# Kernel optimization log

Hardware: AMD Instinct MI355X
Metric: run time of the kernel (lower is better)

## Reference

```python
import jax, jax.numpy as jnp
import numpy as np

COST_CLASS, COST_BBOX, COST_GIOU = 1.0, 5.0, 2.0
BS, Q, K, T = 16, 1024, 256, 128


def setup_inputs() -> dict:
    key = jax.random.key(0)
    k1, k2, k3, k4 = jax.random.split(key, 4)
    pred_logits = jax.random.normal(k1, (BS, Q, K), dtype=jnp.float32)
    # predicted boxes in (mid, width) format, width > 0
    pred_boxes = jax.random.uniform(k2, (BS, Q, 2), dtype=jnp.float32, minval=0.05, maxval=1.0)
    # target boxes in (x0, x1) format with x0 < x1
    tgt_boxes = jnp.sort(jax.random.uniform(k3, (BS, T, 2), dtype=jnp.float32), axis=-1)
    tgt_labels = jax.random.randint(k4, (BS, T), 0, K, dtype=jnp.int32)
    return {"pred_logits": pred_logits, "pred_boxes": pred_boxes,
            "tgt_boxes": tgt_boxes, "tgt_labels": tgt_labels}


def midwtoxy(x):
    mid, w = x[..., 0], x[..., 1]
    return jnp.stack([mid - 0.5 * w, mid + 0.5 * w], axis=-1)


def getgiou(b1, b2):
    # b1: [N,2] (x0,x1), b2: [M,2]; returns [N,M] generalized IoU for 1-D intervals
    area1 = b1[:, 1] - b1[:, 0]              # [N]
    area2 = b2[:, 1] - b2[:, 0]              # [M]
    lt = jnp.maximum(b1[:, None, 0], b2[None, :, 0])
    rb = jnp.minimum(b1[:, None, 1], b2[None, :, 1])
    inter = jnp.clip(rb - lt, 0.0)           # [N,M]
    union = area1[:, None] + area2[None, :] - inter
    iou = inter / union
    hull_lt = jnp.minimum(b1[:, None, 0], b2[None, :, 0])
    hull_rb = jnp.maximum(b1[:, None, 1], b2[None, :, 1])
    hull = jnp.clip(hull_rb - hull_lt, 0.0)
    return iou - (hull - union) / hull


def reference(pred_logits, pred_boxes, tgt_boxes, tgt_labels):
    bs, q, k = pred_logits.shape
    out_prob = jax.nn.softmax(pred_logits.reshape(bs * q, k), axis=-1)  # [bs*Q, K]
    out_bbox = midwtoxy(pred_boxes.reshape(bs * q, 2))                  # [bs*Q, 2] (x0,x1)
    tgt_bbox = tgt_boxes.reshape(-1, 2)                                 # [bs*T, 2]
    tgt_ids = tgt_labels.reshape(-1)                                    # [bs*T]

    cost_class = -out_prob[:, tgt_ids]                                  # [bs*Q, bs*T]
    # L1 cdist over 2 coords, without materializing a [N,M,2] tensor
    cost_bbox = (jnp.abs(out_bbox[:, None, 0] - tgt_bbox[None, :, 0]) +
                 jnp.abs(out_bbox[:, None, 1] - tgt_bbox[None, :, 1]))
    cost_giou = -getgiou(out_bbox, tgt_bbox)

    C = COST_BBOX * cost_bbox + COST_CLASS * cost_class + COST_GIOU * cost_giou
    # [bs, Q, bs*T]; the original feeds the per-sample diagonal blocks
    # C[b, :, b*T:(b+1)*T] to scipy linear_sum_assignment (CPU, non-differentiable,
    # excluded from this GPU-math baseline).
    return C.reshape(bs, q, -1)
```

## Files before the change

### kernel.cpp

```cpp
#include <hip/hip_runtime.h>

#define BS 16
#define Q  1024
#define K  256
#define T  128
#define NROWS (BS * Q)
#define M     (BS * T)
#define RPB   4

__device__ __forceinline__ float cost_fn(float x0, float x1, float w1,
                                         float tx0, float tx1, float p) {
    float l1   = fabsf(x0 - tx0) + fabsf(x1 - tx1);
    float ir   = fminf(x1, tx1) - fmaxf(x0, tx0);
    float s    = w1 + (tx1 - tx0);
    float inter= fmaxf(ir, 0.0f);
    float mn   = fminf(ir, 0.0f);
    float uni  = s - inter;
    float hull = s - ir;
    float giou = (inter * hull + mn * uni) * __builtin_amdgcn_rcpf(uni * hull);
    return fmaf(5.0f, l1, -p) - 2.0f * giou;
}

__global__ __launch_bounds__(256) void hungarian_cost_kernel(
    const float* __restrict__ pred_logits,
    const float* __restrict__ pred_boxes,
    const float* __restrict__ tgt_boxes,
    const int*   __restrict__ tgt_labels,
    float* __restrict__ out)
{
    __shared__ float probs[RPB][K];

    const int t    = threadIdx.x;
    const int w    = t >> 6;
    const int lane = t & 63;
    const int n    = blockIdx.x * RPB + w;

    const float4* lg4 = (const float4*)(pred_logits + (size_t)n * K);
    float4 v = lg4[lane];
    float e0 = __expf(v.x), e1 = __expf(v.y), e2 = __expf(v.z), e3 = __expf(v.w);
    float sum = (e0 + e1) + (e2 + e3);
    #pragma unroll
    for (int off = 1; off < 64; off <<= 1)
        sum += __shfl_xor(sum, off, 64);
    float rs = __builtin_amdgcn_rcpf(sum);

    float4* pr4 = (float4*)&probs[w][0];
    float4 pv; pv.x = e0 * rs; pv.y = e1 * rs; pv.z = e2 * rs; pv.w = e3 * rs;
    pr4[lane] = pv;

    float mid = pred_boxes[(size_t)n * 2 + 0];
    float w1  = pred_boxes[(size_t)n * 2 + 1];
    float x0  = mid - 0.5f * w1;
    float x1  = mid + 0.5f * w1;

    __syncthreads();

    const float4* tb4  = (const float4*)tgt_boxes;
    const int4*   tl4  = (const int4*)tgt_labels;
    float4*       out4 = (float4*)(out + (size_t)n * M);
    const float*  prow = &probs[w][0];

    #pragma unroll
    for (int i = 0; i < 8; ++i) {
        int vv = lane + i * 64;
        float4 b01 = tb4[2 * vv];
        float4 b23 = tb4[2 * vv + 1];
        int4   lab = tl4[vv];

        float4 r;
        r.x = cost_fn(x0, x1, w1, b01.x, b01.y, prow[lab.x]);
        r.y = cost_fn(x0, x1, w1, b01.z, b01.w, prow[lab.y]);
        r.z = cost_fn(x0, x1, w1, b23.x, b23.y, prow[lab.z]);
        r.w = cost_fn(x0, x1, w1, b23.z, b23.w, prow[lab.w]);
        out4[vv] = r;
    }
}

extern "C" void kernel_launch(void* const* d_in, const int* in_sizes, int n_in,
                              void* d_out, int out_size, void* d_ws, size_t ws_size,
                              hipStream_t stream) {
    const float* pred_logits = (const float*)d_in[0];
    const float* pred_boxes  = (const float*)d_in[1];
    const float* tgt_boxes   = (const float*)d_in[2];
    const int*   tgt_labels  = (const int*)d_in[3];
    float* out = (float*)d_out;

    hungarian_cost_kernel<<<NROWS / RPB, 256, 0, stream>>>(
        pred_logits, pred_boxes, tgt_boxes, tgt_labels, out);
}
```

Baseline: 160.1 us.

## Process eight rows per block and reuse target loads across rows

Each block now handles 8 prediction rows, with every wave computing softmax for two rows. Instead of one wave per row, the whole block walks the target columns and each thread loads a target box/label chunk once, then reuses it for all 8 rows held in registers. Target widths are hoisted out of the per-row cost. This cuts redundant global loads of targets and labels. In exchange the grid is halved, register use goes up, and the block needs more shared memory.

```diff
diff --git a/kernel.cpp b/kernel.cpp
--- a/kernel.cpp
+++ b/kernel.cpp
@@ -6,13 +6,14 @@
 #define T  128
 #define NROWS (BS * Q)
 #define M     (BS * T)
-#define RPB   4
+#define RPB   8
 
 __device__ __forceinline__ float cost_fn(float x0, float x1, float w1,
-                                         float tx0, float tx1, float p) {
+                                         float tx0, float tx1, float w2,
+                                         float p) {
     float l1   = fabsf(x0 - tx0) + fabsf(x1 - tx1);
     float ir   = fminf(x1, tx1) - fmaxf(x0, tx0);
-    float s    = w1 + (tx1 - tx0);
+    float s    = w1 + w2;
     float inter= fmaxf(ir, 0.0f);
     float mn   = fminf(ir, 0.0f);
     float uni  = s - inter;
@@ -29,50 +30,68 @@
     float* __restrict__ out)
 {
     __shared__ float probs[RPB][K];
+    __shared__ float rbox[RPB][3];
 
     const int t    = threadIdx.x;
     const int w    = t >> 6;
     const int lane = t & 63;
-    const int n    = blockIdx.x * RPB + w;
+    const int row0 = blockIdx.x * RPB;
 
-    const float4* lg4 = (const float4*)(pred_logits + (size_t)n * K);
-    float4 v = lg4[lane];
-    float e0 = __expf(v.x), e1 = __expf(v.y), e2 = __expf(v.z), e3 = __expf(v.w);
-    float sum = (e0 + e1) + (e2 + e3);
     #pragma unroll
-    for (int off = 1; off < 64; off <<= 1)
-        sum += __shfl_xor(sum, off, 64);
-    float rs = __builtin_amdgcn_rcpf(sum);
-
-    float4* pr4 = (float4*)&probs[w][0];
-    float4 pv; pv.x = e0 * rs; pv.y = e1 * rs; pv.z = e2 * rs; pv.w = e3 * rs;
-    pr4[lane] = pv;
-
-    float mid = pred_boxes[(size_t)n * 2 + 0];
-    float w1  = pred_boxes[(size_t)n * 2 + 1];
-    float x0  = mid - 0.5f * w1;
-    float x1  = mid + 0.5f * w1;
-
+    for (int r = 0; r < 2; ++r) {
+        int lr = 2 * w + r;
+        int n  = row0 + lr;
+        float4 v = ((const float4*)(pred_logits + (size_t)n * K))[lane];
+        float e0 = __expf(v.x), e1 = __expf(v.y), e2 = __expf(v.z), e3 = __expf(v.w);
+        float sum = (e0 + e1) + (e2 + e3);
+        #pragma unroll
+        for (int off = 1; off < 64; off <<= 1)
+            sum += __shfl_xor(sum, off, 64);
+        float rs = __builtin_amdgcn_rcpf(sum);
+        float4 pv; pv.x = e0 * rs; pv.y = e1 * rs; pv.z = e2 * rs; pv.w = e3 * rs;
+        ((float4*)&probs[lr][0])[lane] = pv;
+        if (lane == 0) {
+            float mid = pred_boxes[(size_t)n * 2 + 0];
+            float ww  = pred_boxes[(size_t)n * 2 + 1];
+            rbox[lr][0] = mid - 0.5f * ww;
+            rbox[lr][1] = mid + 0.5f * ww;
+            rbox[lr][2] = ww;
+        }
+    }
     __syncthreads();
 
-    const float4* tb4  = (const float4*)tgt_boxes;
-    const int4*   tl4  = (const int4*)tgt_labels;
-    float4*       out4 = (float4*)(out + (size_t)n * M);
-    const float*  prow = &probs[w][0];
+    float rx0[RPB], rx1[RPB], rw1[RPB];
+    #pragma unroll
+    for (int r = 0; r < RPB; ++r) {
+        rx0[r] = rbox[r][0]; rx1[r] = rbox[r][1]; rw1[r] = rbox[r][2];
+    }
+
+    const float4* tb4 = (const float4*)tgt_boxes;
+    const int4*   tl4 = (const int4*)tgt_labels;
 
     #pragma unroll
-    for (int i = 0; i < 8; ++i) {
-        int vv = lane + i * 64;
+    for (int c = 0; c < 2; ++c) {
+        int vv = t + c * 256;
         float4 b01 = tb4[2 * vv];
         float4 b23 = tb4[2 * vv + 1];
         int4   lab = tl4[vv];
 
-        float4 r;
-        r.x = cost_fn(x0, x1, w1, b01.x, b01.y, prow[lab.x]);
-        r.y = cost_fn(x0, x1, w1, b01.z, b01.w, prow[lab.y]);
-        r.z = cost_fn(x0, x1, w1, b23.x, b23.y, prow[lab.z]);
-        r.w = cost_fn(x0, x1, w1, b23.z, b23.w, prow[lab.w]);
-        out4[vv] = r;
+        float w2a = b01.y - b01.x;
+        float w2b = b01.w - b01.z;
+        float w2c = b23.y - b23.x;
+        float w2d = b23.w - b23.z;
+
+        #pragma unroll
+        for (int r = 0; r < RPB; ++r) {
+            float x0 = rx0[r], x1 = rx1[r], w1 = rw1[r];
+            const float* prow = &probs[r][0];
+            float4 rr;
+            rr.x = cost_fn(x0, x1, w1, b01.x, b01.y, w2a, prow[lab.x]);
+            rr.y = cost_fn(x0, x1, w1, b01.z, b01.w, w2b, prow[lab.y]);
+            rr.z = cost_fn(x0, x1, w1, b23.x, b23.y, w2c, prow[lab.z]);
+            rr.w = cost_fn(x0, x1, w1, b23.z, b23.w, w2d, prow[lab.w]);
+            ((float4*)(out + (size_t)(row0 + r) * M))[vv] = rr;
+        }
     }
 }
 
```

After: 151.5 us. 1.06x faster.
